# Kernel optimization log

Measured on AMD Instinct MI355X. Metric: run time of the kernel, lower is better.

The kernel has to match this reference:

```python
import jax, jax.numpy as jnp
import numpy as np

N_NODES = 100000
N_EDGES = 1600000
D_IN = 64
HIDDEN = 64


def _res_gated_conv(x, Wk, Wq, Wv, Ws, b, src, dst, num_nodes):
    # PyG ResGatedGraphConv: eta_ij = sigmoid(k_i + q_j); out_i = skip(x_i) + sum_j eta_ij * v_j + bias
    k = x @ Wk  # [N, H] keys (applied to target/dst side)
    q = x @ Wq  # [N, H] queries (source side)
    v = x @ Wv  # [N, H] values (source side)
    msg = jax.nn.sigmoid(k[dst] + q[src]) * v[src]  # [E, H] gated messages
    agg = jax.ops.segment_sum(msg, dst, num_segments=num_nodes)  # scatter-add to dst
    return agg + x @ Ws + b


def setup_inputs() -> dict:
    key = jax.random.key(0)
    ks = jax.random.split(key, 16)
    scale_in = 1.0 / np.sqrt(D_IN)
    scale_h = 1.0 / np.sqrt(HIDDEN)

    x = jax.random.normal(ks[0], (N_NODES, D_IN), dtype=jnp.float32)
    edge_index = jax.random.randint(ks[1], (2, N_EDGES), 0, N_NODES, dtype=jnp.int64)

    def w(k, din, dout, s):
        return jax.random.normal(k, (din, dout), dtype=jnp.float32) * s

    inp = {
        "x": x,
        "Wk1": w(ks[2], D_IN, HIDDEN, scale_in),
        "Wq1": w(ks[3], D_IN, HIDDEN, scale_in),
        "Wv1": w(ks[4], D_IN, HIDDEN, scale_in),
        "Ws1": w(ks[5], D_IN, HIDDEN, scale_in),
        "b1": jnp.zeros((HIDDEN,), dtype=jnp.float32),
        "Wl1": w(ks[6], HIDDEN, HIDDEN, scale_h),
        "bl1": jnp.zeros((HIDDEN,), dtype=jnp.float32),
        "Wk2": w(ks[7], HIDDEN, HIDDEN, scale_h),
        "Wq2": w(ks[8], HIDDEN, HIDDEN, scale_h),
        "Wv2": w(ks[9], HIDDEN, HIDDEN, scale_h),
        "Ws2": w(ks[10], HIDDEN, HIDDEN, scale_h),
        "b2": jnp.zeros((HIDDEN,), dtype=jnp.float32),
        "Wl2": w(ks[11], HIDDEN, HIDDEN, scale_h),
        "bl2": jnp.zeros((HIDDEN,), dtype=jnp.float32),
        "edge_index": edge_index,
    }
    return inp


def reference(x, Wk1, Wq1, Wv1, Ws1, b1, Wl1, bl1,
              Wk2, Wq2, Wv2, Ws2, b2, Wl2, bl2, edge_index):
    src, dst = edge_index[0], edge_index[1]
    n = x.shape[0]
    h = _res_gated_conv(x, Wk1, Wq1, Wv1, Ws1, b1, src, dst, n)
    h = jax.nn.relu(h @ Wl1 + bl1)
    h = _res_gated_conv(h, Wk2, Wq2, Wv2, Ws2, b2, src, dst, n)
    h = jax.nn.relu(h @ Wl2 + bl2)
    return h
```

## Files before the change

### kernel.cpp

```cpp
#include <hip/hip_runtime.h>

#define N_NODES 100000
#define N_EDGES 1600000
#define NB      782
#define NSB     (NB * 8)
#define SBCAP   512

typedef unsigned short ushort_t;
typedef unsigned int uint_t;

static __device__ __forceinline__ ushort_t bf16_rne(float f) {
    uint_t u = __float_as_uint(f);
    u = (u + 0x7FFFu + ((u >> 16) & 1u)) >> 16;
    return (ushort_t)u;
}
static __device__ __forceinline__ uint_t bfpack(float lo, float hi) {
    return (uint_t)bf16_rne(lo) | ((uint_t)bf16_rne(hi) << 16);
}
static __device__ __forceinline__ float bf2f(ushort_t h) {
    return __uint_as_float(((uint_t)h) << 16);
}

#define FMA16(A, xv) do { \
    A[0]  = fmaf((xv), wa.x, A[0]);  A[1]  = fmaf((xv), wa.y, A[1]);  \
    A[2]  = fmaf((xv), wa.z, A[2]);  A[3]  = fmaf((xv), wa.w, A[3]);  \
    A[4]  = fmaf((xv), wb.x, A[4]);  A[5]  = fmaf((xv), wb.y, A[5]);  \
    A[6]  = fmaf((xv), wb.z, A[6]);  A[7]  = fmaf((xv), wb.w, A[7]);  \
    A[8]  = fmaf((xv), wc.x, A[8]);  A[9]  = fmaf((xv), wc.y, A[9]);  \
    A[10] = fmaf((xv), wc.z, A[10]); A[11] = fmaf((xv), wc.w, A[11]); \
    A[12] = fmaf((xv), wd.x, A[12]); A[13] = fmaf((xv), wd.y, A[13]); \
    A[14] = fmaf((xv), wd.z, A[14]); A[15] = fmaf((xv), wd.w, A[15]); \
} while (0)

__global__ __launch_bounds__(256) void bucket_kernel(
    const int* __restrict__ EI, int* __restrict__ bcnt, uint_t* __restrict__ bbuf)
{
    int e = blockIdx.x * 256 + threadIdx.x;
    if (e >= N_EDGES) return;
    int s = EI[e];
    int d = EI[N_EDGES + e];
    int sb = (d >> 7) * 8 + (blockIdx.x & 7);
    int p = atomicAdd(&bcnt[sb], 1);
    if (p < SBCAP)
        bbuf[(size_t)sb * SBCAP + p] = (uint_t)s | ((uint_t)(d & 127) << 17);
}

__global__ __launch_bounds__(1024) void bucket_scan_kernel(
    const int* __restrict__ bcnt, int* __restrict__ bbase)
{
    __shared__ int s[1024];
    int tid = threadIdx.x;
    int tot = 0;
    if (tid < NB) {
        #pragma unroll
        for (int j = 0; j < 8; ++j) {
            int c = bcnt[tid * 8 + j];
            tot += (c < SBCAP) ? c : SBCAP;
        }
    }
    s[tid] = tot;
    __syncthreads();
    for (int off = 1; off < 1024; off <<= 1) {
        int t = (tid >= off) ? s[tid - off] : 0;
        __syncthreads();
        s[tid] += t;
        __syncthreads();
    }
    if (tid < NB) bbase[tid] = s[tid] - tot;
}

__global__ __launch_bounds__(256) void csr_kernel(
    const int* __restrict__ bcnt, const uint_t* __restrict__ bbuf,
    const int* __restrict__ bbase,
    int* __restrict__ deg, int* __restrict__ start, int* __restrict__ ssrc)
{
    __shared__ uint_t ebuf[8 * SBCAP];
    __shared__ int cnt[128];
    __shared__ int lst[128];
    __shared__ int scnt[8];
    __shared__ int soff[8];
    const int b = blockIdx.x, tid = threadIdx.x;

    if (tid < 8) {
        int c = bcnt[b * 8 + tid];
        scnt[tid] = (c < SBCAP) ? c : SBCAP;
    }
    if (tid < 128) cnt[tid] = 0;
    __syncthreads();
    if (tid == 0) {
        int r = 0;
        #pragma unroll
        for (int j = 0; j < 8; ++j) { soff[j] = r; r += scnt[j]; }
    }
    __syncthreads();
    const int total = soff[7] + scnt[7];

    for (int j = 0; j < 8; ++j) {
        int c = scnt[j], o = soff[j];
        const uint_t* src = bbuf + (size_t)(b * 8 + j) * SBCAP;
        for (int i = tid; i < c; i += 256) {
            uint_t u = src[i];
            ebuf[o + i] = u;
            atomicAdd(&cnt[(u >> 17) & 127], 1);
        }
    }
    __syncthreads();

    if (tid < 128) lst[tid] = cnt[tid];
    __syncthreads();
    for (int off = 1; off < 128; off <<= 1) {
        int t = (tid < 128 && tid >= off) ? lst[tid - off] : 0;
        __syncthreads();
        if (tid < 128) lst[tid] += t;
        __syncthreads();
    }
    const int base = bbase[b];
    if (tid < 128) {
        lst[tid] -= cnt[tid];
        int n = b * 128 + tid;
        deg[n] = cnt[tid];
        start[n] = base + lst[tid];
        cnt[tid] = 0;
    }
    __syncthreads();

    for (int i = tid; i < total; i += 256) {
        uint_t u = ebuf[i];
        int dl = (u >> 17) & 127;
        int pos = base + lst[dl] + atomicAdd(&cnt[dl], 1);
        ssrc[pos] = (int)(u & 0x1FFFFu);
    }
}

__global__ __launch_bounds__(256) void transform4_kernel(
    const float* __restrict__ X,
    const float* __restrict__ W0, const float* __restrict__ W1,
    const float* __restrict__ W2, const float* __restrict__ W3,
    const float* __restrict__ B3,
    float* __restrict__ K, ushort_t* __restrict__ Qh,
    ushort_t* __restrict__ Vh, float* __restrict__ AGG)
{
    __shared__ float xs[64][65];
    __shared__ float ws[2][64][64];
    const int tid  = threadIdx.x;
    const int base = blockIdx.x * 64;
    const int pair = blockIdx.y;

    {
        const float* WA = pair ? W2 : W0;
        const float* WB = pair ? W3 : W1;
        float4* dA = (float4*)&ws[0][0][0];
        float4* dB = (float4*)&ws[1][0][0];
        for (int i = tid; i < 1024; i += 256) {
            dA[i] = ((const float4*)WA)[i];
            dB[i] = ((const float4*)WB)[i];
        }
    }
    for (int i = tid; i < 1024; i += 256) {
        int r = i >> 4, c = i & 15;
        int node = base + r;
        float4 v = make_float4(0.f, 0.f, 0.f, 0.f);
        if (node < N_NODES) v = ((const float4*)X)[(size_t)node * 16 + c];
        *(float4*)&xs[r][c * 4] = v;
    }
    __syncthreads();

    const int wid    = tid >> 6;
    const int lane   = tid & 63;
    const int matsel = wid >> 1;
    const int lg     = ((wid & 1) << 6) | lane;
    const int ng     = lg >> 2;
    const int og     = (lg & 3) * 16;

    float acc0[16], acc1[16];
    #pragma unroll
    for (int j = 0; j < 16; ++j) { acc0[j] = 0.f; acc1[j] = 0.f; }

    for (int k = 0; k < 64; ++k) {
        float4 wa = *(const float4*)&ws[matsel][k][og + 0];
        float4 wb = *(const float4*)&ws[matsel][k][og + 4];
        float4 wc = *(const float4*)&ws[matsel][k][og + 8];
        float4 wd = *(const float4*)&ws[matsel][k][og + 12];
        float x0 = xs[2 * ng + 0][k];
        float x1 = xs[2 * ng + 1][k];
        FMA16(acc0, x0);
        FMA16(acc1, x1);
    }

    const int kind = pair * 2 + matsel;
    if (kind == 0 || kind == 3) {
        float bias[16];
        #pragma unroll
        for (int j = 0; j < 16; ++j) bias[j] = (kind == 3) ? B3[og + j] : 0.f;
        float* O = (kind == 0) ? K : AGG;
        #pragma unroll
        for (int i = 0; i < 2; ++i) {
            int node = base + 2 * ng + i;
            if (node < N_NODES) {
                float* dst = O + (size_t)node * 64 + og;
                const float* A = (i == 0) ? acc0 : acc1;
                *(float4*)(dst + 0)  = make_float4(A[0]  + bias[0],  A[1]  + bias[1],
                                                   A[2]  + bias[2],  A[3]  + bias[3]);
                *(float4*)(dst + 4)  = make_float4(A[4]  + bias[4],  A[5]  + bias[5],
                                                   A[6]  + bias[6],  A[7]  + bias[7]);
                *(float4*)(dst + 8)  = make_float4(A[8]  + bias[8],  A[9]  + bias[9],
                                                   A[10] + bias[10], A[11] + bias[11]);
                *(float4*)(dst + 12) = make_float4(A[12] + bias[12], A[13] + bias[13],
                                                   A[14] + bias[14], A[15] + bias[15]);
            }
        }
    } else {
        ushort_t* O = (kind == 1) ? Qh : Vh;
        #pragma unroll
        for (int i = 0; i < 2; ++i) {
            int node = base + 2 * ng + i;
            if (node < N_NODES) {
                uint_t* dst = (uint_t*)(O + (size_t)node * 64 + og);
                const float* A = (i == 0) ? acc0 : acc1;
                uint4 u0, u1;
                u0.x = bfpack(A[0],  A[1]);  u0.y = bfpack(A[2],  A[3]);
                u0.z = bfpack(A[4],  A[5]);  u0.w = bfpack(A[6],  A[7]);
                u1.x = bfpack(A[8],  A[9]);  u1.y = bfpack(A[10], A[11]);
                u1.z = bfpack(A[12], A[13]); u1.w = bfpack(A[14], A[15]);
                *(uint4*)(dst + 0) = u0;
                *(uint4*)(dst + 4) = u1;
            }
        }
    }
}

__global__ __launch_bounds__(256) void agg_kernel(
    const float* __restrict__ K, const ushort_t* __restrict__ Qh,
    const ushort_t* __restrict__ Vh, const int* __restrict__ start,
    const int* __restrict__ deg, const int* __restrict__ ssrc,
    float* __restrict__ AGG)
{
    int n = (blockIdx.x * 256 + threadIdx.x) >> 6;
    int lane = threadIdx.x & 63;
    int eg = lane >> 4;
    int c  = (lane & 15) * 4;

    const float4 kv = *(const float4*)(K + (size_t)n * 64 + c);
    float4 acc = make_float4(0.f, 0.f, 0.f, 0.f);

    int s0 = start[n];
    int dn = deg[n];
    for (int p = eg; p < dn; p += 4) {
        int s = ssrc[s0 + p];
        ushort4 qh = *(const ushort4*)(Qh + (size_t)s * 64 + c);
        ushort4 vh = *(const ushort4*)(Vh + (size_t)s * 64 + c);
        float ex = __expf(-(kv.x + bf2f(qh.x)));
        float ey = __expf(-(kv.y + bf2f(qh.y)));
        float ez = __expf(-(kv.z + bf2f(qh.z)));
        float ew = __expf(-(kv.w + bf2f(qh.w)));
        acc.x = fmaf(bf2f(vh.x), __builtin_amdgcn_rcpf(1.f + ex), acc.x);
        acc.y = fmaf(bf2f(vh.y), __builtin_amdgcn_rcpf(1.f + ey), acc.y);
        acc.z = fmaf(bf2f(vh.z), __builtin_amdgcn_rcpf(1.f + ez), acc.z);
        acc.w = fmaf(bf2f(vh.w), __builtin_amdgcn_rcpf(1.f + ew), acc.w);
    }

    acc.x += __shfl_xor(acc.x, 16); acc.y += __shfl_xor(acc.y, 16);
    acc.z += __shfl_xor(acc.z, 16); acc.w += __shfl_xor(acc.w, 16);
    acc.x += __shfl_xor(acc.x, 32); acc.y += __shfl_xor(acc.y, 32);
    acc.z += __shfl_xor(acc.z, 32); acc.w += __shfl_xor(acc.w, 32);

    if (eg == 0) {
        float4* a = (float4*)(AGG + (size_t)n * 64 + c);
        float4 o = *a;
        o.x += acc.x; o.y += acc.y; o.z += acc.z; o.w += acc.w;
        *a = o;
    }
}

__global__ __launch_bounds__(256) void relu_gemm_kernel(
    const float* __restrict__ AGG, const float* __restrict__ WL,
    const float* __restrict__ BL, float* __restrict__ OUT)
{
    __shared__ float xin[64][65];
    __shared__ float wl[64][64];
    const int tid  = threadIdx.x;
    const int base = blockIdx.x * 64;

    {
        float4* dl = (float4*)&wl[0][0];
        for (int i = tid; i < 1024; i += 256) dl[i] = ((const float4*)WL)[i];
    }
    for (int i = tid; i < 1024; i += 256) {
        int r = i >> 4, c = i & 15;
        int node = base + r;
        float4 v = make_float4(0.f, 0.f, 0.f, 0.f);
        if (node < N_NODES) v = ((const float4*)AGG)[(size_t)node * 16 + c];
        *(float4*)&xin[r][c * 4] = v;
    }
    __syncthreads();

    const int node = tid >> 2;
    const int og   = (tid & 3) * 16;
    float acc[16];
    #pragma unroll
    for (int j = 0; j < 16; ++j) acc[j] = 0.f;
    for (int k = 0; k < 64; ++k) {
        float4 wa = *(const float4*)&wl[k][og + 0];
        float4 wb = *(const float4*)&wl[k][og + 4];
        float4 wc = *(const float4*)&wl[k][og + 8];
        float4 wd = *(const float4*)&wl[k][og + 12];
        float xv = xin[node][k];
        FMA16(acc, xv);
    }

    int out_node = base + node;
    if (out_node < N_NODES) {
        float* dst = OUT + (size_t)out_node * 64 + og;
        float r0[16];
        #pragma unroll
        for (int j = 0; j < 16; ++j) r0[j] = fmaxf(acc[j] + BL[og + j], 0.f);
        *(float4*)(dst + 0)  = make_float4(r0[0],  r0[1],  r0[2],  r0[3]);
        *(float4*)(dst + 4)  = make_float4(r0[4],  r0[5],  r0[6],  r0[7]);
        *(float4*)(dst + 8)  = make_float4(r0[8],  r0[9],  r0[10], r0[11]);
        *(float4*)(dst + 12) = make_float4(r0[12], r0[13], r0[14], r0[15]);
    }
}

extern "C" void kernel_launch(void* const* d_in, const int* in_sizes, int n_in,
                              void* d_out, int out_size, void* d_ws, size_t ws_size,
                              hipStream_t stream)
{
    const float* x   = (const float*)d_in[0];
    const float* Wk1 = (const float*)d_in[1];
    const float* Wq1 = (const float*)d_in[2];
    const float* Wv1 = (const float*)d_in[3];
    const float* Ws1 = (const float*)d_in[4];
    const float* b1  = (const float*)d_in[5];
    const float* Wl1 = (const float*)d_in[6];
    const float* bl1 = (const float*)d_in[7];
    const float* Wk2 = (const float*)d_in[8];
    const float* Wq2 = (const float*)d_in[9];
    const float* Wv2 = (const float*)d_in[10];
    const float* Ws2 = (const float*)d_in[11];
    const float* b2  = (const float*)d_in[12];
    const float* Wl2 = (const float*)d_in[13];
    const float* bl2 = (const float*)d_in[14];
    const int*   ei  = (const int*)d_in[15];

    const size_t NF = (size_t)N_NODES * 64;
    float*    K    = (float*)d_ws;
    float*    AGG  = K + NF;
    float*    H    = AGG + NF;
    ushort_t* Qh   = (ushort_t*)(H + NF);
    ushort_t* Vh   = Qh + NF;
    int*      bcnt = (int*)(Vh + NF);
    int*      bbase = bcnt + NSB;
    int*      deg   = bbase + 1024;
    int*      start = deg + 100352;
    int*      ssrc  = start + 100352;
    uint_t*   bbuf  = (uint_t*)(ssrc + N_EDGES);

    hipMemsetAsync(bcnt, 0, NSB * sizeof(int), stream);
    bucket_kernel<<<N_EDGES / 256, 256, 0, stream>>>(ei, bcnt, bbuf);
    bucket_scan_kernel<<<1, 1024, 0, stream>>>(bcnt, bbase);
    csr_kernel<<<NB, 256, 0, stream>>>(bcnt, bbuf, bbase, deg, start, ssrc);

    transform4_kernel<<<dim3(1563, 2), 256, 0, stream>>>(x, Wk1, Wq1, Wv1, Ws1, b1,
                                                         K, Qh, Vh, AGG);
    agg_kernel<<<N_NODES / 4, 256, 0, stream>>>(K, Qh, Vh, start, deg, ssrc, AGG);
    relu_gemm_kernel<<<1563, 256, 0, stream>>>(AGG, Wl1, bl1, H);

    transform4_kernel<<<dim3(1563, 2), 256, 0, stream>>>(H, Wk2, Wq2, Wv2, Ws2, b2,
                                                         K, Qh, Vh, AGG);
    agg_kernel<<<N_NODES / 4, 256, 0, stream>>>(K, Qh, Vh, start, deg, ssrc, AGG);
    relu_gemm_kernel<<<1563, 256, 0, stream>>>(AGG, Wl2, bl2, (float*)d_out);
}
```

Baseline: 511.0 us.

## Replace atomic global bucketing with two-pass histogram, scan and scatter

Edge bucketing into 782 destination buckets moves from a single pass using global atomics into fixed-capacity sub-buckets to a counting sort. One pass builds per-block histograms in shared memory, a column scan computes exact offsets, and a second pass scatters edges into a contiguous buffer. This removes global atomic contention and the memset, and drops the per-sub-bucket cap of 512. The cost is reading the edge list twice, two extra launches, and a single-block serial column scan over 256 rows.

```diff
diff --git a/kernel.cpp b/kernel.cpp
--- a/kernel.cpp
+++ b/kernel.cpp
@@ -3,8 +3,9 @@
 #define N_NODES 100000
 #define N_EDGES 1600000
 #define NB      782
-#define NSB     (NB * 8)
-#define SBCAP   512
+#define NBLK_E  256
+#define CHUNK_E 6250
+#define EBUF_CAP 4096
 
 typedef unsigned short ushort_t;
 typedef unsigned int uint_t;
@@ -32,33 +33,38 @@
     A[14] = fmaf((xv), wd.z, A[14]); A[15] = fmaf((xv), wd.w, A[15]); \
 } while (0)
 
-__global__ __launch_bounds__(256) void bucket_kernel(
-    const int* __restrict__ EI, int* __restrict__ bcnt, uint_t* __restrict__ bbuf)
-{
-    int e = blockIdx.x * 256 + threadIdx.x;
-    if (e >= N_EDGES) return;
-    int s = EI[e];
-    int d = EI[N_EDGES + e];
-    int sb = (d >> 7) * 8 + (blockIdx.x & 7);
-    int p = atomicAdd(&bcnt[sb], 1);
-    if (p < SBCAP)
-        bbuf[(size_t)sb * SBCAP + p] = (uint_t)s | ((uint_t)(d & 127) << 17);
-}
-
-__global__ __launch_bounds__(1024) void bucket_scan_kernel(
-    const int* __restrict__ bcnt, int* __restrict__ bbase)
+__global__ __launch_bounds__(256) void hist782_kernel(
+    const int* __restrict__ EI, int* __restrict__ hmat)
+{
+    __shared__ int h[NB];
+    const int tid = threadIdx.x;
+    for (int i = tid; i < NB; i += 256) h[i] = 0;
+    __syncthreads();
+    const int e0 = blockIdx.x * CHUNK_E;
+    for (int i = tid; i < CHUNK_E; i += 256) {
+        int d = EI[N_EDGES + e0 + i];
+        atomicAdd(&h[d >> 7], 1);
+    }
+    __syncthreads();
+    int* row = hmat + blockIdx.x * NB;
+    for (int i = tid; i < NB; i += 256) row[i] = h[i];
+}
+
+__global__ __launch_bounds__(1024) void colscan_kernel(
+    int* __restrict__ hmat, int* __restrict__ bbase2, int* __restrict__ btot)
 {
     __shared__ int s[1024];
-    int tid = threadIdx.x;
-    int tot = 0;
+    const int tid = threadIdx.x;
+    int run = 0;
     if (tid < NB) {
-        #pragma unroll
-        for (int j = 0; j < 8; ++j) {
-            int c = bcnt[tid * 8 + j];
-            tot += (c < SBCAP) ? c : SBCAP;
+        for (int blk = 0; blk < NBLK_E; ++blk) {
+            int idx = blk * NB + tid;
+            int v = hmat[idx];
+            hmat[idx] = run;
+            run += v;
         }
     }
-    s[tid] = tot;
+    s[tid] = (tid < NB) ? run : 0;
     __syncthreads();
     for (int off = 1; off < 1024; off <<= 1) {
         int t = (tid >= off) ? s[tid - off] : 0;
@@ -66,43 +72,55 @@
         s[tid] += t;
         __syncthreads();
     }
-    if (tid < NB) bbase[tid] = s[tid] - tot;
+    if (tid < NB) {
+        bbase2[tid] = s[tid] - run;
+        btot[tid]   = run;
+    }
+}
+
+__global__ __launch_bounds__(256) void scat782_kernel(
+    const int* __restrict__ EI, const int* __restrict__ hmat,
+    const int* __restrict__ bbase2, uint_t* __restrict__ sbuf)
+{
+    __shared__ int base[NB];
+    __shared__ int cur[NB];
+    const int tid = threadIdx.x;
+    const int* row = hmat + blockIdx.x * NB;
+    for (int i = tid; i < NB; i += 256) {
+        base[i] = bbase2[i] + row[i];
+        cur[i] = 0;
+    }
+    __syncthreads();
+    const int e0 = blockIdx.x * CHUNK_E;
+    for (int i = tid; i < CHUNK_E; i += 256) {
+        int sN = EI[e0 + i];
+        int d  = EI[N_EDGES + e0 + i];
+        int b  = d >> 7;
+        int p  = base[b] + atomicAdd(&cur[b], 1);
+        sbuf[p] = (uint_t)sN | ((uint_t)(d & 127) << 17);
+    }
 }
 
 __global__ __launch_bounds__(256) void csr_kernel(
-    const int* __restrict__ bcnt, const uint_t* __restrict__ bbuf,
-    const int* __restrict__ bbase,
+    const int* __restrict__ bbase2, const int* __restrict__ btot,
+    const uint_t* __restrict__ sbuf,
     int* __restrict__ deg, int* __restrict__ start, int* __restrict__ ssrc)
 {
-    __shared__ uint_t ebuf[8 * SBCAP];
+    __shared__ uint_t ebuf[EBUF_CAP];
     __shared__ int cnt[128];
     __shared__ int lst[128];
-    __shared__ int scnt[8];
-    __shared__ int soff[8];
     const int b = blockIdx.x, tid = threadIdx.x;
-
-    if (tid < 8) {
-        int c = bcnt[b * 8 + tid];
-        scnt[tid] = (c < SBCAP) ? c : SBCAP;
-    }
+    const int base = bbase2[b];
+    int total = btot[b];
+    if (total > EBUF_CAP) total = EBUF_CAP;
+
     if (tid < 128) cnt[tid] = 0;
     __syncthreads();
-    if (tid == 0) {
-        int r = 0;
-        #pragma unroll
-        for (int j = 0; j < 8; ++j) { soff[j] = r; r += scnt[j]; }
-    }
-    __syncthreads();
-    const int total = soff[7] + scnt[7];
-
-    for (int j = 0; j < 8; ++j) {
-        int c = scnt[j], o = soff[j];
-        const uint_t* src = bbuf + (size_t)(b * 8 + j) * SBCAP;
-        for (int i = tid; i < c; i += 256) {
-            uint_t u = src[i];
-            ebuf[o + i] = u;
-            atomicAdd(&cnt[(u >> 17) & 127], 1);
-        }
+
+    for (int i = tid; i < total; i += 256) {
+        uint_t u = sbuf[base + i];
+        ebuf[i] = u;
+        atomicAdd(&cnt[(u >> 17) & 127], 1);
     }
     __syncthreads();
 
@@ -114,7 +132,6 @@
         if (tid < 128) lst[tid] += t;
         __syncthreads();
     }
-    const int base = bbase[b];
     if (tid < 128) {
         lst[tid] -= cnt[tid];
         int n = b * 128 + tid;
@@ -343,22 +360,23 @@
     const int*   ei  = (const int*)d_in[15];
 
     const size_t NF = (size_t)N_NODES * 64;
-    float*    K    = (float*)d_ws;
-    float*    AGG  = K + NF;
-    float*    H    = AGG + NF;
-    ushort_t* Qh   = (ushort_t*)(H + NF);
-    ushort_t* Vh   = Qh + NF;
-    int*      bcnt = (int*)(Vh + NF);
-    int*      bbase = bcnt + NSB;
-    int*      deg   = bbase + 1024;
+    float*    K     = (float*)d_ws;
+    float*    AGG   = K + NF;
+    float*    H     = AGG + NF;
+    ushort_t* Qh    = (ushort_t*)(H + NF);
+    ushort_t* Vh    = Qh + NF;
+    int*      hmat  = (int*)(Vh + NF);
+    int*      bbase2 = hmat + NBLK_E * NB;
+    int*      btot  = bbase2 + 1024;
+    int*      deg   = btot + 1024;
     int*      start = deg + 100352;
     int*      ssrc  = start + 100352;
-    uint_t*   bbuf  = (uint_t*)(ssrc + N_EDGES);
-
-    hipMemsetAsync(bcnt, 0, NSB * sizeof(int), stream);
-    bucket_kernel<<<N_EDGES / 256, 256, 0, stream>>>(ei, bcnt, bbuf);
-    bucket_scan_kernel<<<1, 1024, 0, stream>>>(bcnt, bbase);
-    csr_kernel<<<NB, 256, 0, stream>>>(bcnt, bbuf, bbase, deg, start, ssrc);
+    uint_t*   sbuf  = (uint_t*)(ssrc + N_EDGES);
+
+    hist782_kernel<<<NBLK_E, 256, 0, stream>>>(ei, hmat);
+    colscan_kernel<<<1, 1024, 0, stream>>>(hmat, bbase2, btot);
+    scat782_kernel<<<NBLK_E, 256, 0, stream>>>(ei, hmat, bbase2, sbuf);
+    csr_kernel<<<NB, 256, 0, stream>>>(bbase2, btot, sbuf, deg, start, ssrc);
 
     transform4_kernel<<<dim3(1563, 2), 256, 0, stream>>>(x, Wk1, Wq1, Wv1, Ws1, b1,
                                                          K, Qh, Vh, AGG);
```

Result: faster. 478.5 us (-6.4%).
